# Performance work log

Measured on AMD Instinct MI355X. Metric: run time of the kernel, lower is better.

Reference implementation:

```python
import jax, jax.numpy as jnp
from jax import lax
import numpy as np

B, T, H, C = 64, 512, 1024, 21


def setup_inputs() -> dict:
    key = jax.random.key(0)
    k1, k2, k3, k4 = jax.random.split(key, 4)
    return {
        "sequence_output": jax.random.normal(k1, (B, T, H), dtype=jnp.float32),
        "input_mask": jax.random.randint(k2, (B, T), 0, 2, dtype=jnp.int32),
        "W": jax.random.normal(k3, (H, C), dtype=jnp.float32) * 0.02,
        "b": jnp.zeros((C,), dtype=jnp.float32),
        "transitions": jax.random.normal(k4, (C, C), dtype=jnp.float32) * 0.1,
    }


def crf_decode(logits, transitions, seq_len):
    """Viterbi decode matching tfa.text.crf_decode semantics (length-masked)."""
    Bb, Tt, Cc = logits.shape
    ident = jnp.arange(Cc, dtype=jnp.int32)[None, :]  # identity backpointers

    def fwd_step(state, inp):
        logit_t, t = inp  # [B,C], scalar step index
        scores = state[:, :, None] + transitions[None, :, :]  # [B, C_prev, C_cur]
        bp = jnp.argmax(scores, axis=1).astype(jnp.int32)      # [B, C]
        new_state = jnp.max(scores, axis=1) + logit_t          # [B, C]
        valid = (t < seq_len)[:, None]                          # [B, 1]
        state = jnp.where(valid, new_state, state)
        bp = jnp.where(valid, bp, ident)
        return state, bp

    ts = jnp.arange(1, Tt)
    xs = (jnp.transpose(logits[:, 1:], (1, 0, 2)), ts)
    final_state, bps = lax.scan(fwd_step, logits[:, 0], xs)  # bps: [T-1, B, C]
    last_tag = jnp.argmax(final_state, axis=-1).astype(jnp.int32)  # [B]

    def back_step(tag, bp_t):
        tag = jnp.take_along_axis(bp_t, tag[:, None], axis=1)[:, 0]
        return tag, tag

    _, tags_rev = lax.scan(back_step, last_tag, bps, reverse=True)  # [T-1, B]
    tags = jnp.concatenate([tags_rev, last_tag[None, :]], axis=0)   # [T, B]
    return jnp.transpose(tags, (1, 0))  # [B, T]


def reference(sequence_output, input_mask, W, b, transitions):
    # classifier logits
    logits = jnp.einsum("bth,hc->btc", sequence_output, W) + b  # [B,T,C]
    mask = (input_mask == 1).astype(jnp.int32)
    seq_len = jnp.sum(mask, axis=-1)  # [B]
    decode_tags = crf_decode(logits, transitions, seq_len)
    return jax.nn.one_hot(decode_tags, logits.shape[-1], dtype=jnp.float32), logits
```

## Files before the change

kernel.cpp:

```cpp
#include <hip/hip_runtime.h>
#include <stdint.h>

#define BB 64
#define TT 512
#define HH 1024
#define CC 21

#define GAS __attribute__((address_space(1)))
#define LAS __attribute__((address_space(3)))
__device__ __forceinline__ void gll16(const void* g, void* l) {
    __builtin_amdgcn_global_load_lds((const GAS uint32_t*)g, (LAS uint32_t*)l, 16, 0, 0);
}

#define RL(x, lane) __uint_as_float(__builtin_amdgcn_readlane(__float_as_uint(x), (lane)))

__global__ __launch_bounds__(512) void logits_split_kernel(
    const float* __restrict__ seq,
    const float* __restrict__ W,
    const float* __restrict__ bias,
    float* __restrict__ outA,
    float* __restrict__ outB)
{
    __shared__ float comb[7][128][22];

    const int t = threadIdx.x;
    const int w = t >> 6;
    const int l = t & 63;
    const int r  = blockIdx.x >> 1;
    const int hb = blockIdx.x & 1;
    const int row0 = r * 128;
    const int h0 = hb * 512 + w * 64;

    const float* x0 = seq + (size_t)(row0 + l) * HH + h0;
    const float* x1 = seq + (size_t)(row0 + l + 64) * HH + h0;
    const float* wb = W + (size_t)h0 * CC;

    float acc0[CC], acc1[CC];
#pragma unroll
    for (int c = 0; c < CC; ++c) { acc0[c] = 0.f; acc1[c] = 0.f; }

    float4 xa[4], xbv[4], xan[4], xbn[4];
    float wr[6], wrn[6];

#pragma unroll
    for (int k = 0; k < 4; ++k) {
        xa[k]  = *(const float4*)(x0 + k * 4);
        xbv[k] = *(const float4*)(x1 + k * 4);
    }
#pragma unroll
    for (int i = 0; i < 6; ++i) {
        int j = i * 64 + l;
        wr[i] = (j < 16 * CC) ? wb[j] : 0.f;
    }

#pragma unroll 2
    for (int ch = 0; ch < 4; ++ch) {
        if (ch < 3) {
            const float* px0 = x0 + (ch + 1) * 16;
            const float* px1 = x1 + (ch + 1) * 16;
#pragma unroll
            for (int k = 0; k < 4; ++k) {
                xan[k] = *(const float4*)(px0 + k * 4);
                xbn[k] = *(const float4*)(px1 + k * 4);
            }
            const float* pw = wb + (ch + 1) * 16 * CC;
#pragma unroll
            for (int i = 0; i < 6; ++i) {
                int j = i * 64 + l;
                wrn[i] = (j < 16 * CC) ? pw[j] : 0.f;
            }
        }

#pragma unroll
        for (int g = 0; g < 4; ++g) {
#pragma unroll
            for (int j = 0; j < 4; ++j) {
                float xv0 = (&xa[g].x)[j];
                float xv1 = (&xbv[g].x)[j];
#pragma unroll
                for (int c = 0; c < CC; ++c) {
                    const int idx = (g * 4 + j) * CC + c;
                    float s = RL(wr[idx >> 6], idx & 63);
                    acc0[c] = fmaf(s, xv0, acc0[c]);
                    acc1[c] = fmaf(s, xv1, acc1[c]);
                }
            }
        }

        if (ch < 3) {
#pragma unroll
            for (int k = 0; k < 4; ++k) { xa[k] = xan[k]; xbv[k] = xbn[k]; }
#pragma unroll
            for (int i = 0; i < 6; ++i) wr[i] = wrn[i];
        }
    }

    if (w > 0) {
#pragma unroll
        for (int c = 0; c < CC; ++c) {
            comb[w - 1][l][c]      = acc0[c];
            comb[w - 1][l + 64][c] = acc1[c];
        }
    }
    __syncthreads();
    if (w == 0) {
        float* dst = hb ? outB : outA;
        float* o0 = dst + (size_t)(row0 + l) * CC;
        float* o1 = dst + (size_t)(row0 + l + 64) * CC;
#pragma unroll
        for (int c = 0; c < CC; ++c) {
            float s0 = acc0[c] + (hb ? 0.f : bias[c]);
            float s1 = acc1[c] + (hb ? 0.f : bias[c]);
#pragma unroll
            for (int i = 0; i < 7; ++i) {
                s0 += comb[i][l][c];
                s1 += comb[i][l + 64][c];
            }
            o0[c] = s0;
            o1[c] = s1;
        }
    }
}

__global__ __launch_bounds__(512) void logits_full_kernel(
    const float* __restrict__ seq, const float* __restrict__ W,
    const float* __restrict__ bias, float* __restrict__ logits)
{
    __shared__ float comb[7][128][22];
    const int t = threadIdx.x;
    const int w = t >> 6;
    const int l = t & 63;
    const int row0 = blockIdx.x * 128;
    const int h0 = w * 128;

    const float* x0 = seq + (size_t)(row0 + l) * HH + h0;
    const float* x1 = seq + (size_t)(row0 + l + 64) * HH + h0;
    const float* wb = W + (size_t)h0 * CC;

    float acc0[CC], acc1[CC];
#pragma unroll
    for (int c = 0; c < CC; ++c) { acc0[c] = 0.f; acc1[c] = 0.f; }

    float4 xa[4], xbv[4], xan[4], xbn[4];
    float wr[6], wrn[6];
#pragma unroll
    for (int k = 0; k < 4; ++k) {
        xa[k]  = *(const float4*)(x0 + k * 4);
        xbv[k] = *(const float4*)(x1 + k * 4);
    }
#pragma unroll
    for (int i = 0; i < 6; ++i) {
        int j = i * 64 + l;
        wr[i] = (j < 16 * CC) ? wb[j] : 0.f;
    }
#pragma unroll 2
    for (int ch = 0; ch < 8; ++ch) {
        if (ch < 7) {
            const float* px0 = x0 + (ch + 1) * 16;
            const float* px1 = x1 + (ch + 1) * 16;
#pragma unroll
            for (int k = 0; k < 4; ++k) {
                xan[k] = *(const float4*)(px0 + k * 4);
                xbn[k] = *(const float4*)(px1 + k * 4);
            }
            const float* pw = wb + (ch + 1) * 16 * CC;
#pragma unroll
            for (int i = 0; i < 6; ++i) {
                int j = i * 64 + l;
                wrn[i] = (j < 16 * CC) ? pw[j] : 0.f;
            }
        }
#pragma unroll
        for (int g = 0; g < 4; ++g) {
#pragma unroll
            for (int j = 0; j < 4; ++j) {
                float xv0 = (&xa[g].x)[j];
                float xv1 = (&xbv[g].x)[j];
#pragma unroll
                for (int c = 0; c < CC; ++c) {
                    const int idx = (g * 4 + j) * CC + c;
                    float s = RL(wr[idx >> 6], idx & 63);
                    acc0[c] = fmaf(s, xv0, acc0[c]);
                    acc1[c] = fmaf(s, xv1, acc1[c]);
                }
            }
        }
        if (ch < 7) {
#pragma unroll
            for (int k = 0; k < 4; ++k) { xa[k] = xan[k]; xbv[k] = xbn[k]; }
#pragma unroll
            for (int i = 0; i < 6; ++i) wr[i] = wrn[i];
        }
    }
    if (w > 0) {
#pragma unroll
        for (int c = 0; c < CC; ++c) {
            comb[w - 1][l][c]      = acc0[c];
            comb[w - 1][l + 64][c] = acc1[c];
        }
    }
    __syncthreads();
    if (w == 0) {
        float* o0 = logits + (size_t)(row0 + l) * CC;
        float* o1 = logits + (size_t)(row0 + l + 64) * CC;
#pragma unroll
        for (int c = 0; c < CC; ++c) {
            float s0 = acc0[c] + bias[c];
            float s1 = acc1[c] + bias[c];
#pragma unroll
            for (int i = 0; i < 7; ++i) {
                s0 += comb[i][l][c];
                s1 += comb[i][l + 64][c];
            }
            o0[c] = s0;
            o1[c] = s1;
        }
    }
}

__global__ __launch_bounds__(256) void viterbi_kernel(
    const float* __restrict__ logitsA,
    const float* __restrict__ logitsB,
    const int* __restrict__ mask,
    const float* __restrict__ trans,
    float* __restrict__ onehot,
    float* __restrict__ logits_out)
{
    __shared__ __align__(16) float lg[(TT + 1) * CC];
    __shared__ float stS[TT * CC];
    __shared__ float trL[CC * CC];
    __shared__ unsigned char bp[TT * CC];
    __shared__ unsigned char tagl[TT];
    __shared__ unsigned char mapl[12 * CC];
    __shared__ unsigned char bnd[13];

    const int tid = threadIdx.x;
    const int w = tid >> 6;
    const int l = tid & 63;
    const int b = blockIdx.x;

    const float* lb = logitsA + (size_t)b * TT * CC;
    for (int i = w; i < 42; i += 4)
        gll16(lb + (size_t)(i * 64 + l) * 4, &lg[i * 256]);

    float4 bfr[11];
    if (logitsB) {
        const float4* pb = (const float4*)(logitsB + (size_t)b * TT * CC);
#pragma unroll
        for (int k = 0; k < 11; ++k) {
            int j = tid + k * 256;
            bfr[k] = (j < 2688) ? pb[j] : float4{0.f, 0.f, 0.f, 0.f};
        }
    }

    for (int j = tid; j < CC * CC; j += 256) trL[j] = trans[j];

    int sl = 0;
#pragma unroll
    for (int k = 0; k < 8; ++k) sl += mask[b * TT + k * 64 + l];
#pragma unroll
    for (int o = 32; o > 0; o >>= 1) sl += __shfl_xor(sl, o);
    const int idstart = (sl >= 1) ? (sl - 1) : 0;

    asm volatile("s_waitcnt vmcnt(0)" ::: "memory");
    __syncthreads();

    if (logitsB) {
        float4* lg4 = (float4*)lg;
        float4* gout = (float4*)(logits_out + (size_t)b * TT * CC);
#pragma unroll
        for (int k = 0; k < 11; ++k) {
            int j = tid + k * 256;
            if (j < 2688) {
                float4 a = lg4[j];
                a.x += bfr[k].x; a.y += bfr[k].y;
                a.z += bfr[k].z; a.w += bfr[k].w;
                lg4[j] = a;
                gout[j] = a;
            }
        }
        __syncthreads();
    }

    if (w == 0) {
        const bool act = (l < CC);
        const int cc = act ? l : 0;
        float tcol[CC];
#pragma unroll
        for (int cp = 0; cp < CC; ++cp) tcol[cp] = trL[cp * CC + cc];

        float st = lg[cc];
        if (act) stS[l] = st;
        float lgt_next = lg[CC + cc];

#pragma unroll 1
        for (int t = 1; t < sl; ++t) {
            float lgt = lgt_next;
            lgt_next = lg[(t + 1) * CC + cc];
            float sc[CC];
#pragma unroll
            for (int cp = 0; cp < CC; ++cp) sc[cp] = RL(st, cp) + tcol[cp];
            float m0 = fmaxf(fmaxf(sc[0], sc[1]), sc[2]);
            float m1 = fmaxf(fmaxf(sc[3], sc[4]), sc[5]);
            float m2 = fmaxf(fmaxf(sc[6], sc[7]), sc[8]);
            float m3 = fmaxf(fmaxf(sc[9], sc[10]), sc[11]);
            float m4 = fmaxf(fmaxf(sc[12], sc[13]), sc[14]);
            float m5 = fmaxf(fmaxf(sc[15], sc[16]), sc[17]);
            float m6 = fmaxf(fmaxf(sc[18], sc[19]), sc[20]);
            float n0 = fmaxf(fmaxf(m0, m1), m2);
            float n1 = fmaxf(fmaxf(m3, m4), m5);
            float best = fmaxf(fmaxf(n0, n1), m6);
            st = best + lgt;
            if (act) stS[t * CC + l] = st;
        }

        float fs[CC];
#pragma unroll
        for (int cp = 0; cp < CC; ++cp) fs[cp] = RL(st, cp);
        float q0 = fmaxf(fmaxf(fs[0], fs[1]), fs[2]);
        float q1 = fmaxf(fmaxf(fs[3], fs[4]), fs[5]);
        float q2 = fmaxf(fmaxf(fs[6], fs[7]), fs[8]);
        float q3 = fmaxf(fmaxf(fs[9], fs[10]), fs[11]);
        float q4 = fmaxf(fmaxf(fs[12], fs[13]), fs[14]);
        float q5 = fmaxf(fmaxf(fs[15], fs[16]), fs[17]);
        float q6 = fmaxf(fmaxf(fs[18], fs[19]), fs[20]);
        float fbest = fmaxf(fmaxf(fmaxf(q0, q1), fmaxf(q2, q3)),
                            fmaxf(fmaxf(q4, q5), q6));
        int e[CC];
#pragma unroll
        for (int cp = 0; cp < CC; ++cp) e[cp] = (fs[cp] == fbest) ? cp : 63;
        int i0 = min(min(e[0], e[1]), e[2]);
        int i1 = min(min(e[3], e[4]), e[5]);
        int i2 = min(min(e[6], e[7]), e[8]);
        int i3 = min(min(e[9], e[10]), e[11]);
        int i4 = min(min(e[12], e[13]), e[14]);
        int i5 = min(min(e[15], e[16]), e[17]);
        int i6 = min(min(e[18], e[19]), e[20]);
        int last = min(min(min(i0, i1), min(i2, i3)), min(min(i4, i5), i6));
        if (l == 0) tagl[TT - 1] = (unsigned char)last;
    } else {
        int s = (w - 1) * 64 + l;
        if (s < 189) {
            int c0 = s % CC, prow = s / CC;
#pragma unroll 1
            for (int p = idstart + prow; p < TT; p += 9)
                bp[p * CC + c0] = (unsigned char)c0;
        }
    }
    __syncthreads();

    if (tid < 252) {
        const int c0 = tid % CC, tg = tid / CC;
        float tc[CC];
#pragma unroll
        for (int cp = 0; cp < CC; ++cp) tc[cp] = trL[cp * CC + c0];
#pragma unroll 1
        for (int t = 1 + tg; t < sl; t += 12) {
            const float* sp = stS + (t - 1) * CC;
            float bv = sp[0] + tc[0];
            int bi = 0;
#pragma unroll
            for (int cp = 1; cp < CC; ++cp) {
                float v = sp[cp] + tc[cp];
                bool g = v > bv;
                bv = g ? v : bv;
                bi = g ? cp : bi;
            }
            bp[(t - 1) * CC + c0] = (unsigned char)bi;
        }
    }
    __syncthreads();

    if (tid < 252) {
        int g = tid / CC, cand = tid % CC;
        int endp = g * 43;
        int startp = min(g * 43 + 42, TT - 2);
        int m = cand;
#pragma unroll 1
        for (int i = 0; i < 43; ++i) {
            int p = startp - i;
            int pr = (p >= endp) ? p : endp;
            int m2 = bp[pr * CC + m];
            m = (p >= endp) ? m2 : m;
        }
        mapl[g * CC + cand] = (unsigned char)m;
    }
    __syncthreads();

    if (tid == 0) {
        int eb = tagl[TT - 1];
        bnd[12] = (unsigned char)eb;
        for (int g = 11; g >= 0; --g) {
            eb = mapl[g * CC + eb];
            bnd[g] = (unsigned char)eb;
        }
    }
    __syncthreads();

    if (tid < 12) {
        int g = tid;
        int endp = g * 43;
        int startp = min(g * 43 + 42, TT - 2);
        int eb = bnd[g + 1];
#pragma unroll 1
        for (int p = startp; p >= endp; --p) {
            eb = bp[p * CC + eb];
            tagl[p] = (unsigned char)eb;
        }
    }
    __syncthreads();

    if (tid < 252) {
        const int c0 = tid % CC, prow = tid / CC;
        float* ob = onehot + (size_t)b * TT * CC;
#pragma unroll 1
        for (int p = prow; p < TT; p += 12)
            ob[(size_t)p * CC + c0] = (c0 == (int)tagl[p]) ? 1.f : 0.f;
    }
}

extern "C" void kernel_launch(void* const* d_in, const int* in_sizes, int n_in,
                              void* d_out, int out_size, void* d_ws, size_t ws_size,
                              hipStream_t stream) {
    const float* seq   = (const float*)d_in[0];
    const int*   msk   = (const int*)d_in[1];
    const float* W     = (const float*)d_in[2];
    const float* bias  = (const float*)d_in[3];
    const float* trans = (const float*)d_in[4];

    float* onehot_out = (float*)d_out;
    float* logits_out = onehot_out + (size_t)BB * TT * CC;

    const size_t bbytes = (size_t)BB * TT * CC * sizeof(float);
    if (ws_size >= bbytes) {
        float* partB = (float*)d_ws;
        logits_split_kernel<<<512, 512, 0, stream>>>(seq, W, bias,
                                                     logits_out, partB);
        viterbi_kernel<<<BB, 256, 0, stream>>>(logits_out, partB, msk, trans,
                                               onehot_out, logits_out);
    } else {
        logits_full_kernel<<<256, 512, 0, stream>>>(seq, W, bias, logits_out);
        viterbi_kernel<<<BB, 256, 0, stream>>>(logits_out, nullptr, msk, trans,
                                               onehot_out, logits_out);
    }
}
```

Measured before the change: 152.1 us.

## Use tree reduction for cross-wave partial sums and move split partials to workspace

Replaces the single-wave serial reduction of eight wave partials through LDS with a three-level tree reduction, shrinking the shared buffer from 7 to 4 slots. The smaller LDS footprint may allow higher occupancy and spreads the final adds across waves, at the cost of four extra block barriers. Both split partials now go to workspace instead of one going into the output buffer. This needs twice the workspace, and the split path is skipped if that much is not available.

```diff
diff --git a/kernel.cpp b/kernel.cpp
--- a/kernel.cpp
+++ b/kernel.cpp
@@ -21,7 +21,7 @@
     float* __restrict__ outA,
     float* __restrict__ outB)
 {
-    __shared__ float comb[7][128][22];
+    __shared__ float comb[4][128][22];
 
     const int t = threadIdx.x;
     const int w = t >> 6;
@@ -95,11 +95,43 @@
         }
     }
 
-    if (w > 0) {
-#pragma unroll
-        for (int c = 0; c < CC; ++c) {
-            comb[w - 1][l][c]      = acc0[c];
-            comb[w - 1][l + 64][c] = acc1[c];
+    if (w >= 4) {
+#pragma unroll
+        for (int c = 0; c < CC; ++c) {
+            comb[w - 4][l][c]      = acc0[c];
+            comb[w - 4][l + 64][c] = acc1[c];
+        }
+    }
+    __syncthreads();
+    if (w < 4) {
+#pragma unroll
+        for (int c = 0; c < CC; ++c) {
+            acc0[c] += comb[w][l][c];
+            acc1[c] += comb[w][l + 64][c];
+        }
+    }
+    __syncthreads();
+    if (w == 2 || w == 3) {
+#pragma unroll
+        for (int c = 0; c < CC; ++c) {
+            comb[w - 2][l][c]      = acc0[c];
+            comb[w - 2][l + 64][c] = acc1[c];
+        }
+    }
+    __syncthreads();
+    if (w < 2) {
+#pragma unroll
+        for (int c = 0; c < CC; ++c) {
+            acc0[c] += comb[w][l][c];
+            acc1[c] += comb[w][l + 64][c];
+        }
+    }
+    __syncthreads();
+    if (w == 1) {
+#pragma unroll
+        for (int c = 0; c < CC; ++c) {
+            comb[0][l][c]      = acc0[c];
+            comb[0][l + 64][c] = acc1[c];
         }
     }
     __syncthreads();
@@ -109,15 +141,8 @@
         float* o1 = dst + (size_t)(row0 + l + 64) * CC;
 #pragma unroll
         for (int c = 0; c < CC; ++c) {
-            float s0 = acc0[c] + (hb ? 0.f : bias[c]);
-            float s1 = acc1[c] + (hb ? 0.f : bias[c]);
-#pragma unroll
-            for (int i = 0; i < 7; ++i) {
-                s0 += comb[i][l][c];
-                s1 += comb[i][l + 64][c];
-            }
-            o0[c] = s0;
-            o1[c] = s1;
+            o0[c] = acc0[c] + comb[0][l][c]      + (hb ? 0.f : bias[c]);
+            o1[c] = acc1[c] + comb[0][l + 64][c] + (hb ? 0.f : bias[c]);
         }
     }
 }
@@ -126,7 +151,7 @@
     const float* __restrict__ seq, const float* __restrict__ W,
     const float* __restrict__ bias, float* __restrict__ logits)
 {
-    __shared__ float comb[7][128][22];
+    __shared__ float comb[4][128][22];
     const int t = threadIdx.x;
     const int w = t >> 6;
     const int l = t & 63;
@@ -192,11 +217,43 @@
             for (int i = 0; i < 6; ++i) wr[i] = wrn[i];
         }
     }
-    if (w > 0) {
-#pragma unroll
-        for (int c = 0; c < CC; ++c) {
-            comb[w - 1][l][c]      = acc0[c];
-            comb[w - 1][l + 64][c] = acc1[c];
+    if (w >= 4) {
+#pragma unroll
+        for (int c = 0; c < CC; ++c) {
+            comb[w - 4][l][c]      = acc0[c];
+            comb[w - 4][l + 64][c] = acc1[c];
+        }
+    }
+    __syncthreads();
+    if (w < 4) {
+#pragma unroll
+        for (int c = 0; c < CC; ++c) {
+            acc0[c] += comb[w][l][c];
+            acc1[c] += comb[w][l + 64][c];
+        }
+    }
+    __syncthreads();
+    if (w == 2 || w == 3) {
+#pragma unroll
+        for (int c = 0; c < CC; ++c) {
+            comb[w - 2][l][c]      = acc0[c];
+            comb[w - 2][l + 64][c] = acc1[c];
+        }
+    }
+    __syncthreads();
+    if (w < 2) {
+#pragma unroll
+        for (int c = 0; c < CC; ++c) {
+            acc0[c] += comb[w][l][c];
+            acc1[c] += comb[w][l + 64][c];
+        }
+    }
+    __syncthreads();
+    if (w == 1) {
+#pragma unroll
+        for (int c = 0; c < CC; ++c) {
+            comb[0][l][c]      = acc0[c];
+            comb[0][l + 64][c] = acc1[c];
         }
     }
     __syncthreads();
@@ -205,22 +262,15 @@
         float* o1 = logits + (size_t)(row0 + l + 64) * CC;
 #pragma unroll
         for (int c = 0; c < CC; ++c) {
-            float s0 = acc0[c] + bias[c];
-            float s1 = acc1[c] + bias[c];
-#pragma unroll
-            for (int i = 0; i < 7; ++i) {
-                s0 += comb[i][l][c];
-                s1 += comb[i][l + 64][c];
-            }
-            o0[c] = s0;
-            o1[c] = s1;
+            o0[c] = acc0[c] + comb[0][l][c]      + bias[c];
+            o1[c] = acc1[c] + comb[0][l + 64][c] + bias[c];
         }
     }
 }
 
 __global__ __launch_bounds__(256) void viterbi_kernel(
-    const float* __restrict__ logitsA,
-    const float* __restrict__ logitsB,
+    const float* __restrict__ partA,
+    const float* __restrict__ partB,
     const int* __restrict__ mask,
     const float* __restrict__ trans,
     float* __restrict__ onehot,
@@ -239,13 +289,13 @@
     const int l = tid & 63;
     const int b = blockIdx.x;
 
-    const float* lb = logitsA + (size_t)b * TT * CC;
+    const float* lb = partA + (size_t)b * TT * CC;
     for (int i = w; i < 42; i += 4)
         gll16(lb + (size_t)(i * 64 + l) * 4, &lg[i * 256]);
 
     float4 bfr[11];
-    if (logitsB) {
-        const float4* pb = (const float4*)(logitsB + (size_t)b * TT * CC);
+    if (partB) {
+        const float4* pb = (const float4*)(partB + (size_t)b * TT * CC);
 #pragma unroll
         for (int k = 0; k < 11; ++k) {
             int j = tid + k * 256;
@@ -265,7 +315,7 @@
     asm volatile("s_waitcnt vmcnt(0)" ::: "memory");
     __syncthreads();
 
-    if (logitsB) {
+    if (partB) {
         float4* lg4 = (float4*)lg;
         float4* gout = (float4*)(logits_out + (size_t)b * TT * CC);
 #pragma unroll
@@ -431,12 +481,12 @@
     float* onehot_out = (float*)d_out;
     float* logits_out = onehot_out + (size_t)BB * TT * CC;
 
-    const size_t bbytes = (size_t)BB * TT * CC * sizeof(float);
-    if (ws_size >= bbytes) {
-        float* partB = (float*)d_ws;
-        logits_split_kernel<<<512, 512, 0, stream>>>(seq, W, bias,
-                                                     logits_out, partB);
-        viterbi_kernel<<<BB, 256, 0, stream>>>(logits_out, partB, msk, trans,
+    const size_t pbytes = (size_t)BB * TT * CC * sizeof(float);
+    if (ws_size >= 2 * pbytes) {
+        float* partA = (float*)d_ws;
+        float* partB = partA + (size_t)BB * TT * CC;
+        logits_split_kernel<<<512, 512, 0, stream>>>(seq, W, bias, partA, partB);
+        viterbi_kernel<<<BB, 256, 0, stream>>>(partA, partB, msk, trans,
                                                onehot_out, logits_out);
     } else {
         logits_full_kernel<<<256, 512, 0, stream>>>(seq, W, bias, logits_out);
```

New measurement: 150.6 us. About the same (-0.9%).
